# Kernel optimization log

Hardware: AMD Instinct MI355X
Metric: run time of the kernel (lower is better)

Reference implementation:

```python
import jax, jax.numpy as jnp
import numpy as np

N_C = 50000
N_N = 50000
E = 500000
D = 128


def _graph_conv(x_src, src, dst, n_src, n_dst, W, b):
    # DGL GraphConv, norm='both': symmetric degree normalization, then linear.
    ones = jnp.ones(src.shape, x_src.dtype)
    deg_out = jax.ops.segment_sum(ones, src, num_segments=n_src)
    deg_in = jax.ops.segment_sum(ones, dst, num_segments=n_dst)
    norm_src = jnp.maximum(deg_out, 1.0) ** -0.5  # [n_src]
    norm_dst = jnp.maximum(deg_in, 1.0) ** -0.5   # [n_dst]
    m = (x_src * norm_src[:, None])[src]          # [E, D] gather
    agg = jax.ops.segment_sum(m, dst, num_segments=n_dst)  # [n_dst, D]
    return (agg * norm_dst[:, None]) @ W + b


def _sage_conv(x_src, x_dst, src, dst, n_dst, W_self, W_neigh, b):
    # DGL SAGEConv, aggregator='mean': fc_self(h_dst) + fc_neigh(mean_neigh) + bias.
    ones = jnp.ones(src.shape, x_src.dtype)
    deg_in = jnp.maximum(jax.ops.segment_sum(ones, dst, num_segments=n_dst), 1.0)
    h_neigh = jax.ops.segment_sum(x_src[src], dst, num_segments=n_dst) / deg_in[:, None]
    return x_dst @ W_self + h_neigh @ W_neigh + b


def setup_inputs() -> dict:
    key = jax.random.key(0)
    ks = jax.random.split(key, 20)
    s = 1.0 / np.sqrt(D)
    inp = {
        'feat_C': jax.random.normal(ks[0], (N_C, D), jnp.float32),
        'feat_N': jax.random.normal(ks[1], (N_N, D), jnp.float32),
        'W1_cc': jax.random.normal(ks[2], (D, D), jnp.float32) * s,
        'b1_cc': jnp.zeros((D,), jnp.float32),
        'W1_cn': jax.random.normal(ks[3], (D, D), jnp.float32) * s,
        'b1_cn': jnp.zeros((D,), jnp.float32),
        'W1_self': jax.random.normal(ks[4], (D, D), jnp.float32) * s,
        'W1_neigh': jax.random.normal(ks[5], (D, D), jnp.float32) * s,
        'b1_nn': jnp.zeros((D,), jnp.float32),
        'W2_cc': jax.random.normal(ks[6], (D, D), jnp.float32) * s,
        'b2_cc': jnp.zeros((D,), jnp.float32),
        'W2_cn': jax.random.normal(ks[7], (D, D), jnp.float32) * s,
        'b2_cn': jnp.zeros((D,), jnp.float32),
        'W2_self': jax.random.normal(ks[8], (D, D), jnp.float32) * s,
        'W2_neigh': jax.random.normal(ks[9], (D, D), jnp.float32) * s,
        'b2_nn': jnp.zeros((D,), jnp.float32),
        'cc_src': jax.random.randint(ks[10], (E,), 0, N_C),
        'cc_dst': jax.random.randint(ks[11], (E,), 0, N_C),
        'cn_src': jax.random.randint(ks[12], (E,), 0, N_C),
        'cn_dst': jax.random.randint(ks[13], (E,), 0, N_N),
        'nn_src': jax.random.randint(ks[14], (E,), 0, N_N),
        'nn_dst': jax.random.randint(ks[15], (E,), 0, N_N),
    }
    return inp


def reference(feat_C, feat_N, W1_cc, b1_cc, W1_cn, b1_cn, W1_self, W1_neigh, b1_nn,
              W2_cc, b2_cc, W2_cn, b2_cn, W2_self, W2_neigh, b2_nn,
              cc_src, cc_dst, cn_src, cn_dst, nn_src, nn_dst):
    # layer 1 (HeteroGraphConv, aggregate='sum') + relu
    hC = _graph_conv(feat_C, cc_src, cc_dst, N_C, N_C, W1_cc, b1_cc)
    hN = (_graph_conv(feat_C, cn_src, cn_dst, N_C, N_N, W1_cn, b1_cn)
          + _sage_conv(feat_N, feat_N, nn_src, nn_dst, N_N, W1_self, W1_neigh, b1_nn))
    hC = jax.nn.relu(hC)
    hN = jax.nn.relu(hN)
    # layer 2
    oC = _graph_conv(hC, cc_src, cc_dst, N_C, N_C, W2_cc, b2_cc)
    oN = (_graph_conv(hC, cn_src, cn_dst, N_C, N_N, W2_cn, b2_cn)
          + _sage_conv(hN, hN, nn_src, nn_dst, N_N, W2_self, W2_neigh, b2_nn))
    return oC, oN
```

## Files before the change

### kernel.cpp

```cpp
#include <hip/hip_runtime.h>

#define NCN 50000
#define NE  500000
#define DF  128

#define BSHIFT 9
#define NBUCK 98
#define BK 128
#define CAP 7168
#define CHUNK 4096

typedef __attribute__((ext_vector_type(8))) short mfrag;
typedef __attribute__((ext_vector_type(4))) float facc4;

__device__ inline ushort f2bf(float x) {
    unsigned u = __float_as_uint(x);
    unsigned r = (u + 0x7FFFu + ((u >> 16) & 1u)) >> 16;
    return (ushort)r;
}
__device__ inline float bf2f(ushort h) { return __uint_as_float(((unsigned)h) << 16); }

__device__ inline void store_split4m(ushort* __restrict__ T, int row, int lane4,
                                     float4 v, int mode) {
    ushort h0 = f2bf(v.x); ushort l0 = f2bf(v.x - bf2f(h0));
    ushort h1 = f2bf(v.y); ushort l1 = f2bf(v.y - bf2f(h1));
    ushort h2 = f2bf(v.z); ushort l2 = f2bf(v.z - bf2f(h2));
    ushort h3 = f2bf(v.w); ushort l3 = f2bf(v.w - bf2f(h3));
    uint2 hp = make_uint2((uint)h0 | ((uint)h1 << 16), (uint)h2 | ((uint)h3 << 16));
    uint2 lp = make_uint2((uint)l0 | ((uint)l1 << 16), (uint)l2 | ((uint)l3 << 16));
    size_t hiOff, loOff;
    if (mode == 0) { hiOff = (size_t)row * DF; loOff = (size_t)NCN * DF + (size_t)row * DF; }
    else           { hiOff = (size_t)row * 256; loOff = hiOff + 128; }
    *(uint2*)(T + hiOff + lane4 * 4) = hp;
    *(uint2*)(T + loOff + lane4 * 4) = lp;
}

__global__ __launch_bounds__(256) void hist2_k(
    const int* __restrict__ cc_src, const int* __restrict__ cn_src,
    int* __restrict__ cnt2)
{
    int i = blockIdx.x * 256 + threadIdx.x;
    if (i >= NE) return;
    atomicAdd(&cnt2[cc_src[i]], 1);
    atomicAdd(&cnt2[NCN + cn_src[i]], 1);
}

__global__ __launch_bounds__(256) void srcnorm_k(
    const int* __restrict__ cnt2, float* __restrict__ snorm2, int n2)
{
    int i = blockIdx.x * 256 + threadIdx.x;
    if (i >= n2) return;
    int c = cnt2[i]; if (c < 1) c = 1;
    snorm2[i] = rsqrtf((float)c);
}

__global__ __launch_bounds__(256) void binA_k(
    const int* __restrict__ cc_src, const int* __restrict__ cc_dst,
    const int* __restrict__ cn_src, const int* __restrict__ cn_dst,
    const int* __restrict__ nn_src, const int* __restrict__ nn_dst,
    uint2* __restrict__ R, int* __restrict__ bc)
{
    const int s = blockIdx.y;
    const int* key; const int* pay;
    switch (s) {
      case 0: key = cc_dst; pay = cc_src; break;
      case 1: key = cn_dst; pay = cn_src; break;
      default: key = nn_dst; pay = nn_src; break;
    }
    __shared__ uint2 rec[CHUNK];
    __shared__ int lhist[BK], lofs[BK], lcur[BK], gbase[BK];
    __shared__ int ls[256];
    const int tid = threadIdx.x;
    const int base = blockIdx.x * CHUNK;

    int k[16], p[16];
    #pragma unroll
    for (int j = 0; j < 16; ++j) {
        int e = base + j * 256 + tid;
        bool valid = (e < NE);
        k[j] = valid ? key[e] : -1;
        p[j] = valid ? pay[e] : 0;
    }
    if (tid < BK) lhist[tid] = 0;
    __syncthreads();
    #pragma unroll
    for (int j = 0; j < 16; ++j)
        if (k[j] >= 0) atomicAdd(&lhist[k[j] >> BSHIFT], 1);
    __syncthreads();
    int v = (tid < BK) ? lhist[tid] : 0;
    ls[tid] = v;
    __syncthreads();
    #pragma unroll
    for (int off = 1; off < 128; off <<= 1) {
        int t = (tid >= off) ? ls[tid - off] : 0;
        __syncthreads();
        ls[tid] += t;
        __syncthreads();
    }
    if (tid < BK) { int e = ls[tid] - v; lofs[tid] = e; lcur[tid] = e; }
    __syncthreads();
    #pragma unroll
    for (int j = 0; j < 16; ++j) {
        if (k[j] >= 0) {
            int b = k[j] >> BSHIFT;
            int pos = atomicAdd(&lcur[b], 1);
            rec[pos] = make_uint2((unsigned)k[j], (unsigned)p[j]);
        }
    }
    __syncthreads();
    if (tid < BK) {
        int c = lcur[tid] - lofs[tid];
        gbase[tid] = (c > 0) ? atomicAdd(&bc[s * BK + tid], c) : 0;
    }
    __syncthreads();
    int total = ls[127];
    for (int i = tid; i < total; i += 256) {
        uint2 r = rec[i];
        int b = (int)(r.x >> BSHIFT);
        int gi = gbase[b] + (i - lofs[b]);
        R[((size_t)s * NBUCK + b) * CAP + gi] = r;
    }
}

__global__ __launch_bounds__(256) void binB_k(
    const uint2* __restrict__ R, const int* __restrict__ bc,
    int* __restrict__ rp3, int* __restrict__ col3)
{
    const int b = blockIdx.x;
    const int s = blockIdx.y;
    const int tid = threadIdx.x;
    __shared__ int cnt[512];
    __shared__ int lofs[512];
    __shared__ int ls[256];
    __shared__ int sbase;

    const int nrec = bc[s * BK + b];
    const uint2* rec = R + ((size_t)s * NBUCK + b) * CAP;

    for (int i = tid; i < 512; i += 256) cnt[i] = 0;
    __syncthreads();
    for (int i = tid; i < nrec; i += 256)
        atomicAdd(&cnt[rec[i].x & 511], 1);
    __syncthreads();

    {
        int v = (tid < b) ? bc[s * BK + tid] : 0;
        ls[tid] = v;
        __syncthreads();
        for (int off = 128; off > 0; off >>= 1) {
            if (tid < off) ls[tid] += ls[tid + off];
            __syncthreads();
        }
        if (tid == 0) sbase = ls[0];
        __syncthreads();
    }
    const int colBase = sbase;

    int v0 = cnt[2 * tid], v1 = cnt[2 * tid + 1];
    int pairSum = v0 + v1;
    ls[tid] = pairSum;
    __syncthreads();
    #pragma unroll
    for (int off = 1; off < 256; off <<= 1) {
        int t = (tid >= off) ? ls[tid - off] : 0;
        __syncthreads();
        ls[tid] += t;
        __syncthreads();
    }
    int excl = ls[tid] - pairSum;
    lofs[2 * tid] = excl;
    lofs[2 * tid + 1] = excl + v0;
    __syncthreads();
    const int total = ls[255];

    int* rp = rp3 + (size_t)s * (NCN + 1);
    for (int j = tid; j < 512; j += 256) {
        int d = b * 512 + j;
        if (d < NCN) rp[d] = colBase + lofs[j];
    }
    if (b == NBUCK - 1 && tid == 0) rp[NCN] = colBase + total;
    __syncthreads();

    int* col = col3 + (size_t)s * NE + colBase;
    for (int i = tid; i < nrec; i += 256) {
        uint2 r = rec[i];
        int pos = atomicAdd(&lofs[r.x & 511], 1);
        col[pos] = (int)r.y;
    }
}

__global__ __launch_bounds__(256) void wconv_k(
    const float* __restrict__ Wm0, const float* __restrict__ Wm1,
    const float* __restrict__ Wm2, const float* __restrict__ Wm3,
    const float* __restrict__ Wm4, const float* __restrict__ Wm5,
    const float* __restrict__ Wm6, const float* __restrict__ Wm7,
    ushort* __restrict__ out)
{
    const float* Ws[8] = {Wm0, Wm1, Wm2, Wm3, Wm4, Wm5, Wm6, Wm7};
    const float* W = Ws[blockIdx.x];
    ushort* o = out + (size_t)blockIdx.x * 32768;
    for (int i = threadIdx.x; i < 16384; i += 256) {
        int c = i >> 13;
        int r = i & 8191;
        int n = r >> 6;
        int jj = r & 63;
        int kk = c * 64 + (jj ^ ((n & 7) << 3));
        float wv = W[kk * 128 + n];
        ushort h = f2bf(wv);
        float lv = wv - bf2f(h);
        o[c * 16384 + r] = h;
        o[c * 16384 + 8192 + r] = f2bf(lv);
    }
}

__global__ __launch_bounds__(256) void agg_k(
    const float* __restrict__ X0, const int* __restrict__ rp0,
    const int* __restrict__ col0, const float* __restrict__ sc0,
    ushort* __restrict__ out0, int m0,
    const float* __restrict__ X1, const int* __restrict__ rp1,
    const int* __restrict__ col1, const float* __restrict__ sc1,
    ushort* __restrict__ out1, int m1,
    const float* __restrict__ X2, const int* __restrict__ rp2,
    const int* __restrict__ col2, const float* __restrict__ sc2,
    ushort* __restrict__ out2, int m2)
{
    const float* X; const int* rp; const int* col; const float* sc; ushort* out; int mode;
    if (blockIdx.y == 0)      { X = X0; rp = rp0; col = col0; sc = sc0; out = out0; mode = m0; }
    else if (blockIdx.y == 1) { X = X1; rp = rp1; col = col1; sc = sc1; out = out1; mode = m1; }
    else                      { X = X2; rp = rp2; col = col2; sc = sc2; out = out2; mode = m2; }

    int wid = (blockIdx.x * 256 + threadIdx.x) >> 6;
    int half = (threadIdx.x >> 5) & 1;
    int lane4 = threadIdx.x & 31;
    int row = wid * 2 + half;
    if (row >= NCN) return;
    int e0 = rp[row], e1 = rp[row + 1];
    const bool useSc = (sc != nullptr);
    float4 a = make_float4(0.f, 0.f, 0.f, 0.f);
    int e = e0;
    while (e < e1) {
        int cnt = e1 - e; if (cnt > 32) cnt = 32;
        int myc = (lane4 < cnt) ? col[e + lane4] : 0;
        float mysc = (useSc && lane4 < cnt) ? sc[myc] : 1.0f;
        int j = 0;
        for (; j + 4 <= cnt; j += 4) {
            int s0 = __shfl(myc, j, 32),     s1 = __shfl(myc, j + 1, 32);
            int s2 = __shfl(myc, j + 2, 32), s3 = __shfl(myc, j + 3, 32);
            float c0 = __shfl(mysc, j, 32),     c1 = __shfl(mysc, j + 1, 32);
            float c2 = __shfl(mysc, j + 2, 32), c3 = __shfl(mysc, j + 3, 32);
            const float4 u0 = *(const float4*)(X + (size_t)s0 * DF + lane4 * 4);
            const float4 u1 = *(const float4*)(X + (size_t)s1 * DF + lane4 * 4);
            const float4 u2 = *(const float4*)(X + (size_t)s2 * DF + lane4 * 4);
            const float4 u3 = *(const float4*)(X + (size_t)s3 * DF + lane4 * 4);
            a.x = fmaf(u0.x, c0, a.x); a.y = fmaf(u0.y, c0, a.y);
            a.z = fmaf(u0.z, c0, a.z); a.w = fmaf(u0.w, c0, a.w);
            a.x = fmaf(u1.x, c1, a.x); a.y = fmaf(u1.y, c1, a.y);
            a.z = fmaf(u1.z, c1, a.z); a.w = fmaf(u1.w, c1, a.w);
            a.x = fmaf(u2.x, c2, a.x); a.y = fmaf(u2.y, c2, a.y);
            a.z = fmaf(u2.z, c2, a.z); a.w = fmaf(u2.w, c2, a.w);
            a.x = fmaf(u3.x, c3, a.x); a.y = fmaf(u3.y, c3, a.y);
            a.z = fmaf(u3.z, c3, a.z); a.w = fmaf(u3.w, c3, a.w);
        }
        for (; j < cnt; ++j) {
            int s0 = __shfl(myc, j, 32);
            float c0 = __shfl(mysc, j, 32);
            const float4 u0 = *(const float4*)(X + (size_t)s0 * DF + lane4 * 4);
            a.x = fmaf(u0.x, c0, a.x); a.y = fmaf(u0.y, c0, a.y);
            a.z = fmaf(u0.z, c0, a.z); a.w = fmaf(u0.w, c0, a.w);
        }
        e += cnt;
    }
    int deg = e1 - e0; if (deg < 1) deg = 1;
    float dsc = useSc ? rsqrtf((float)deg) : (1.0f / (float)deg);
    a.x *= dsc; a.y *= dsc; a.z *= dsc; a.w *= dsc;
    store_split4m(out, row, lane4, a, mode);
}

template<int NSRC, bool RELU, int F32S, bool A1INT>
__device__ __forceinline__ void gemm_body(
    ushort* __restrict__ Wsm,
    const void* __restrict__ A0, const void* __restrict__ A1, const void* __restrict__ A2,
    const ushort* __restrict__ Wi0, const ushort* __restrict__ Wi1, const ushort* __restrict__ Wi2,
    const float* __restrict__ b0, const float* __restrict__ b1,
    float* __restrict__ Y)
{
    constexpr int NCH = 2 * NSRC;
    const int tid = threadIdx.x;
    const int l = tid & 63;
    const int wv = tid >> 6;
    const int r0 = blockIdx.x * 128;
    const int M = NCN;

    const void*   Aarr[3] = {A0, A1, A2};
    const ushort* Warr[3] = {Wi0, Wi1, Wi2};

    int arow[2];
    #pragma unroll
    for (int rt = 0; rt < 2; ++rt) {
        int r = r0 + wv * 32 + rt * 16 + (l & 15);
        arow[rt] = (r < M) ? r : (M - 1);
    }
    const int kgrp = (l >> 4) * 8;

    facc4 acc[2][8];
    #pragma unroll
    for (int rt = 0; rt < 2; ++rt)
        #pragma unroll
        for (int ct = 0; ct < 8; ++ct)
            acc[rt][ct] = (facc4){0.f, 0.f, 0.f, 0.f};

    uint4 Wr[8];
    auto loadWr = [&](int c) {
        int s = c >> 1, chalf = c & 1;
        const uint4* wp = (const uint4*)(Warr[s] + chalf * 16384);
        #pragma unroll
        for (int i = 0; i < 8; ++i) Wr[i] = wp[i * 256 + tid];
    };

    mfrag ah[2][2], al[2][2];
    auto loadA = [&](int c) {
        int s = c >> 1;
        int k0 = (c & 1) * 64;
        if (s == F32S) {
            const float* F = (const float*)Aarr[s];
            #pragma unroll
            for (int ks = 0; ks < 2; ++ks)
                #pragma unroll
                for (int rt = 0; rt < 2; ++rt) {
                    const float* p = F + (size_t)arow[rt] * DF + k0 + ks * 32 + kgrp;
                    float4 v0 = *(const float4*)p;
                    float4 v1 = *(const float4*)(p + 4);
                    union { mfrag m; ushort u[8]; } H, L;
                    float vv0[4] = {v0.x, v0.y, v0.z, v0.w};
                    float vv1[4] = {v1.x, v1.y, v1.z, v1.w};
                    #pragma unroll
                    for (int j = 0; j < 4; ++j) {
                        ushort h = f2bf(vv0[j]);
                        H.u[j] = h; L.u[j] = f2bf(vv0[j] - bf2f(h));
                    }
                    #pragma unroll
                    for (int j = 0; j < 4; ++j) {
                        ushort h = f2bf(vv1[j]);
                        H.u[4 + j] = h; L.u[4 + j] = f2bf(vv1[j] - bf2f(h));
                    }
                    ah[ks][rt] = H.m; al[ks][rt] = L.m;
                }
        } else {
            const ushort* T = (const ushort*)Aarr[s];
            const bool INT = (s == 1 && A1INT);
            const int rs = INT ? 256 : DF;
            const size_t lo = INT ? 128 : (size_t)NCN * DF;
            #pragma unroll
            for (int ks = 0; ks < 2; ++ks)
                #pragma unroll
                for (int rt = 0; rt < 2; ++rt) {
                    size_t o = (size_t)arow[rt] * rs + k0 + ks * 32 + kgrp;
                    ah[ks][rt] = *(const mfrag*)(T + o);
                    al[ks][rt] = *(const mfrag*)(T + o + lo);
                }
        }
    };

    loadWr(0);
    #pragma unroll
    for (int c = 0; c < NCH; ++c) {
        __syncthreads();
        {
            uint4* wd = (uint4*)Wsm;
            #pragma unroll
            for (int i = 0; i < 8; ++i) wd[i * 256 + tid] = Wr[i];
        }
        loadA(c);
        if (c + 1 < NCH) loadWr(c + 1);
        __syncthreads();
        #pragma unroll
        for (int ks = 0; ks < 2; ++ks) {
            const int kbyte = ks * 64 + (l >> 4) * 16;
            #pragma unroll
            for (int ct = 0; ct < 8; ++ct) {
                int colc = ct * 16 + (l & 15);
                int widx = colc * 64 + ((kbyte ^ ((colc & 7) << 4)) >> 1);
                mfrag w_hi = *(const mfrag*)(Wsm + widx);
                mfrag w_lo = *(const mfrag*)(Wsm + 8192 + widx);
                #pragma unroll
                for (int rt = 0; rt < 2; ++rt) {
                    acc[rt][ct] = __builtin_amdgcn_mfma_f32_16x16x32_bf16(ah[ks][rt], w_hi, acc[rt][ct], 0, 0, 0);
                    acc[rt][ct] = __builtin_amdgcn_mfma_f32_16x16x32_bf16(ah[ks][rt], w_lo, acc[rt][ct], 0, 0, 0);
                    acc[rt][ct] = __builtin_amdgcn_mfma_f32_16x16x32_bf16(al[ks][rt], w_hi, acc[rt][ct], 0, 0, 0);
                }
            }
        }
    }
    __syncthreads();

    float bias[8];
    #pragma unroll
    for (int ct = 0; ct < 8; ++ct) {
        int colc = ct * 16 + (l & 15);
        float bv = b0 ? b0[colc] : 0.f;
        if (b1) bv += b1[colc];
        bias[ct] = bv;
    }
    #pragma unroll
    for (int rt = 0; rt < 2; ++rt) {
        #pragma unroll
        for (int q = 0; q < 4; ++q) {
            int row = r0 + wv * 32 + rt * 16 + (l >> 4) * 4 + q;
            if (row < M) {
                #pragma unroll
                for (int ct = 0; ct < 8; ++ct) {
                    float v = acc[rt][ct][q] + bias[ct];
                    if (RELU) v = fmaxf(v, 0.f);
                    Y[(size_t)row * DF + ct * 16 + (l & 15)] = v;
                }
            }
        }
    }
}

template<bool RELU>
__global__ __launch_bounds__(256, 2) void fgemm2_k(
    const ushort* __restrict__ AN0, const ushort* __restrict__ AN1i,
    const float* __restrict__ AN2f,
    const ushort* __restrict__ WiN0, const ushort* __restrict__ WiN1,
    const ushort* __restrict__ WiN2,
    const float* __restrict__ bN0, const float* __restrict__ bN1,
    float* __restrict__ YN,
    const ushort* __restrict__ AC0, const ushort* __restrict__ WiC,
    const float* __restrict__ bC, float* __restrict__ YC)
{
    __shared__ ushort Wsm[16384];
    if (blockIdx.z == 0)
        gemm_body<3, RELU, 2, true>(Wsm, AN0, AN1i, AN2f, WiN0, WiN1, WiN2,
                                    bN0, bN1, YN);
    else
        gemm_body<1, RELU, -1, false>(Wsm, AC0, nullptr, nullptr,
                                      WiC, nullptr, nullptr, bC, nullptr, YC);
}

template<bool RELU>
__global__ __launch_bounds__(256, 2) void gemmN_k(
    const ushort* __restrict__ A0, const ushort* __restrict__ A1i,
    const float* __restrict__ A2f,
    const ushort* __restrict__ Wi0, const ushort* __restrict__ Wi1,
    const ushort* __restrict__ Wi2,
    const float* __restrict__ b0, const float* __restrict__ b1,
    float* __restrict__ Y)
{
    __shared__ ushort Wsm[16384];
    gemm_body<3, RELU, 2, true>(Wsm, A0, A1i, A2f, Wi0, Wi1, Wi2, b0, b1, Y);
}

template<bool RELU>
__global__ __launch_bounds__(256, 2) void gemmC_k(
    const ushort* __restrict__ A0, const ushort* __restrict__ Wi0,
    const float* __restrict__ b0, float* __restrict__ Y)
{
    __shared__ ushort Wsm[16384];
    gemm_body<1, RELU, -1, false>(Wsm, A0, nullptr, nullptr, Wi0, nullptr, nullptr,
                                  b0, nullptr, Y);
}

extern "C" void kernel_launch(void* const* d_in, const int* in_sizes, int n_in,
                              void* d_out, int out_size, void* d_ws, size_t ws_size,
                              hipStream_t stream)
{
    (void)in_sizes; (void)n_in; (void)out_size; (void)ws_size;
    const float* feat_C   = (const float*)d_in[0];
    const float* feat_N   = (const float*)d_in[1];
    const float* W1_cc    = (const float*)d_in[2];
    const float* b1_cc    = (const float*)d_in[3];
    const float* W1_cn    = (const float*)d_in[4];
    const float* b1_cn    = (const float*)d_in[5];
    const float* W1_self  = (const float*)d_in[6];
    const float* W1_neigh = (const float*)d_in[7];
    const float* b1_nn    = (const float*)d_in[8];
    const float* W2_cc    = (const float*)d_in[9];
    const float* b2_cc    = (const float*)d_in[10];
    const float* W2_cn    = (const float*)d_in[11];
    const float* b2_cn    = (const float*)d_in[12];
    const float* W2_self  = (const float*)d_in[13];
    const float* W2_neigh = (const float*)d_in[14];
    const float* b2_nn    = (const float*)d_in[15];
    const int* cc_src = (const int*)d_in[16];
    const int* cc_dst = (const int*)d_in[17];
    const int* cn_src = (const int*)d_in[18];
    const int* cn_dst = (const int*)d_in[19];
    const int* nn_src = (const int*)d_in[20];
    const int* nn_dst = (const int*)d_in[21];

    char* ws = (char*)d_ws;
    size_t off = 0;
    auto take = [&](size_t bytes) -> char* {
        char* p = ws + off;
        off = (off + bytes + 255) & ~(size_t)255;
        return p;
    };
    int*    rp3    = (int*)take((size_t)3 * (NCN + 1) * sizeof(int));
    int*    col3   = (int*)take((size_t)3 * NE * sizeof(int));
    float*  snorm2 = (float*)take((size_t)2 * NCN * sizeof(float));
    int*    cnt2   = (int*)take((size_t)2 * NCN * sizeof(int));
    int*    bc     = (int*)take((size_t)3 * BK * sizeof(int));
    ushort* Wimg   = (ushort*)take((size_t)8 * 32768 * sizeof(ushort));
    char* bigRegion = take((size_t)2 * 2 * NCN * DF * sizeof(ushort));
    uint2*  R  = (uint2*)bigRegion;
    ushort* P0 = (ushort*)bigRegion;
    ushort* P1 = (ushort*)(bigRegion + (size_t)2 * NCN * DF * sizeof(ushort));

    float* oC = (float*)d_out;
    float* oN = oC + (size_t)NCN * DF;
    ushort* oC_us = (ushort*)oC;
    ushort* oN_us = (ushort*)oN;

    const int edgeBlocks = (NE + 255) / 256;
    const int binABlocks = (NE + CHUNK - 1) / CHUNK;
    const int aggBlocks  = (((NCN + 1) / 2) * 64 + 255) / 256;
    const int gemmBlocks = (NCN + 127) / 128;

    auto img = [&](int m) { return (const ushort*)(Wimg + (size_t)m * 32768); };
    const int* rpCC = rp3 + 0 * (NCN + 1);
    const int* rpCN = rp3 + 1 * (NCN + 1);
    const int* rpNN = rp3 + 2 * (NCN + 1);
    const int* colCC = col3 + 0 * NE;
    const int* colCN = col3 + 1 * NE;
    const int* colNN = col3 + 2 * NE;
    const float* snCC = snorm2 + 0 * NCN;
    const float* snCN = snorm2 + 1 * NCN;

    hipMemsetAsync(cnt2, 0, (size_t)2 * NCN * sizeof(int), stream);
    hipMemsetAsync(bc, 0, (size_t)3 * BK * sizeof(int), stream);
    hist2_k<<<edgeBlocks, 256, 0, stream>>>(cc_src, cn_src, cnt2);
    srcnorm_k<<<(2 * NCN + 255) / 256, 256, 0, stream>>>(cnt2, snorm2, 2 * NCN);
    binA_k<<<dim3(binABlocks, 3), 256, 0, stream>>>(cc_src, cc_dst, cn_src, cn_dst,
                                                    nn_src, nn_dst, R, bc);
    binB_k<<<dim3(NBUCK, 3), 256, 0, stream>>>(R, bc, rp3, col3);
    wconv_k<<<8, 256, 0, stream>>>(W1_cc, W1_cn, W1_neigh, W1_self,
                                   W2_cc, W2_cn, W2_neigh, W2_self, Wimg);

    agg_k<<<dim3(aggBlocks, 3), 256, 0, stream>>>(
        feat_C, rpCC, colCC, snCC, P0, 0,
        feat_C, rpCN, colCN, snCN, P1, 0,
        feat_N, rpNN, colNN, nullptr, oN_us, 1);
    fgemm2_k<true><<<dim3(gemmBlocks, 1, 2), 256, 0, stream>>>(
        P1, oN_us, feat_N, img(1), img(2), img(3), b1_cn, b1_nn, oN,
        P0, img(0), b1_cc, oC);

    agg_k<<<dim3(aggBlocks, 2), 256, 0, stream>>>(
        oC, rpCC, colCC, snCC, P0, 0,
        oC, rpCN, colCN, snCN, P1, 0,
        nullptr, nullptr, nullptr, nullptr, nullptr, 0);
    agg_k<<<dim3(aggBlocks, 1), 256, 0, stream>>>(
        oN, rpNN, colNN, nullptr, oC_us, 1,
        nullptr, nullptr, nullptr, nullptr, nullptr, 0,
        nullptr, nullptr, nullptr, nullptr, nullptr, 0);
    gemmN_k<false><<<gemmBlocks, 256, 0, stream>>>(P1, oC_us, oN,
                                                   img(5), img(6), img(7),
                                                   b2_cn, b2_nn, oN);
    gemmC_k<false><<<gemmBlocks, 256, 0, stream>>>(P0, img(4), b2_cc, oC);
}
```

Measured before the change: 425.7 us.

## Use a third workspace table to fuse layer-2 aggregations and GEMMs

When the workspace has room, the neighbour-mean aggregation for the NN relation is written to a separate P2 buffer instead of aliasing the output. Layer 2 can then run all three aggregations in one launch and both GEMMs in one fused launch, cutting the launch count from four to two. Launch bounds on the GEMM kernels also rise from 2 to 3 blocks per CU, which can force register spilling. The extra buffer costs workspace memory, and the old path is kept as a fallback.

```diff
diff --git a/kernel.cpp b/kernel.cpp
--- a/kernel.cpp
+++ b/kernel.cpp
@@ -418,9 +418,9 @@
     }
 }
 
-template<bool RELU>
-__global__ __launch_bounds__(256, 2) void fgemm2_k(
-    const ushort* __restrict__ AN0, const ushort* __restrict__ AN1i,
+template<bool RELU, bool A1INT>
+__global__ __launch_bounds__(256, 3) void fgemm2_k(
+    const ushort* __restrict__ AN0, const ushort* __restrict__ AN1,
     const float* __restrict__ AN2f,
     const ushort* __restrict__ WiN0, const ushort* __restrict__ WiN1,
     const ushort* __restrict__ WiN2,
@@ -431,15 +431,15 @@
 {
     __shared__ ushort Wsm[16384];
     if (blockIdx.z == 0)
-        gemm_body<3, RELU, 2, true>(Wsm, AN0, AN1i, AN2f, WiN0, WiN1, WiN2,
-                                    bN0, bN1, YN);
+        gemm_body<3, RELU, 2, A1INT>(Wsm, AN0, AN1, AN2f, WiN0, WiN1, WiN2,
+                                     bN0, bN1, YN);
     else
         gemm_body<1, RELU, -1, false>(Wsm, AC0, nullptr, nullptr,
                                       WiC, nullptr, nullptr, bC, nullptr, YC);
 }
 
 template<bool RELU>
-__global__ __launch_bounds__(256, 2) void gemmN_k(
+__global__ __launch_bounds__(256, 3) void gemmN_k(
     const ushort* __restrict__ A0, const ushort* __restrict__ A1i,
     const float* __restrict__ A2f,
     const ushort* __restrict__ Wi0, const ushort* __restrict__ Wi1,
@@ -452,7 +452,7 @@
 }
 
 template<bool RELU>
-__global__ __launch_bounds__(256, 2) void gemmC_k(
+__global__ __launch_bounds__(256, 3) void gemmC_k(
     const ushort* __restrict__ A0, const ushort* __restrict__ Wi0,
     const float* __restrict__ b0, float* __restrict__ Y)
 {
@@ -465,7 +465,7 @@
                               void* d_out, int out_size, void* d_ws, size_t ws_size,
                               hipStream_t stream)
 {
-    (void)in_sizes; (void)n_in; (void)out_size; (void)ws_size;
+    (void)in_sizes; (void)n_in; (void)out_size;
     const float* feat_C   = (const float*)d_in[0];
     const float* feat_N   = (const float*)d_in[1];
     const float* W1_cc    = (const float*)d_in[2];
@@ -496,16 +496,19 @@
         off = (off + bytes + 255) & ~(size_t)255;
         return p;
     };
+    const size_t TBL = (size_t)2 * NCN * DF * sizeof(ushort);
     int*    rp3    = (int*)take((size_t)3 * (NCN + 1) * sizeof(int));
     int*    col3   = (int*)take((size_t)3 * NE * sizeof(int));
     float*  snorm2 = (float*)take((size_t)2 * NCN * sizeof(float));
     int*    cnt2   = (int*)take((size_t)2 * NCN * sizeof(int));
     int*    bc     = (int*)take((size_t)3 * BK * sizeof(int));
     ushort* Wimg   = (ushort*)take((size_t)8 * 32768 * sizeof(ushort));
-    char* bigRegion = take((size_t)2 * 2 * NCN * DF * sizeof(ushort));
+    char* bigRegion = take(2 * TBL);
     uint2*  R  = (uint2*)bigRegion;
     ushort* P0 = (ushort*)bigRegion;
-    ushort* P1 = (ushort*)(bigRegion + (size_t)2 * NCN * DF * sizeof(ushort));
+    ushort* P1 = (ushort*)(bigRegion + TBL);
+    const bool useP2 = (ws_size >= off + TBL);
+    ushort* P2 = useP2 ? (ushort*)take(TBL) : nullptr;
 
     float* oC = (float*)d_out;
     float* oN = oC + (size_t)NCN * DF;
@@ -537,24 +540,40 @@
     wconv_k<<<8, 256, 0, stream>>>(W1_cc, W1_cn, W1_neigh, W1_self,
                                    W2_cc, W2_cn, W2_neigh, W2_self, Wimg);
 
-    agg_k<<<dim3(aggBlocks, 3), 256, 0, stream>>>(
-        feat_C, rpCC, colCC, snCC, P0, 0,
-        feat_C, rpCN, colCN, snCN, P1, 0,
-        feat_N, rpNN, colNN, nullptr, oN_us, 1);
-    fgemm2_k<true><<<dim3(gemmBlocks, 1, 2), 256, 0, stream>>>(
-        P1, oN_us, feat_N, img(1), img(2), img(3), b1_cn, b1_nn, oN,
-        P0, img(0), b1_cc, oC);
-
-    agg_k<<<dim3(aggBlocks, 2), 256, 0, stream>>>(
-        oC, rpCC, colCC, snCC, P0, 0,
-        oC, rpCN, colCN, snCN, P1, 0,
-        nullptr, nullptr, nullptr, nullptr, nullptr, 0);
-    agg_k<<<dim3(aggBlocks, 1), 256, 0, stream>>>(
-        oN, rpNN, colNN, nullptr, oC_us, 1,
-        nullptr, nullptr, nullptr, nullptr, nullptr, 0,
-        nullptr, nullptr, nullptr, nullptr, nullptr, 0);
-    gemmN_k<false><<<gemmBlocks, 256, 0, stream>>>(P1, oC_us, oN,
-                                                   img(5), img(6), img(7),
-                                                   b2_cn, b2_nn, oN);
-    gemmC_k<false><<<gemmBlocks, 256, 0, stream>>>(P0, img(4), b2_cc, oC);
-}
+    if (useP2) {
+        agg_k<<<dim3(aggBlocks, 3), 256, 0, stream>>>(
+            feat_C, rpCC, colCC, snCC, P0, 0,
+            feat_C, rpCN, colCN, snCN, P1, 0,
+            feat_N, rpNN, colNN, nullptr, P2, 0);
+        fgemm2_k<true, false><<<dim3(gemmBlocks, 1, 2), 256, 0, stream>>>(
+            P1, P2, feat_N, img(1), img(2), img(3), b1_cn, b1_nn, oN,
+            P0, img(0), b1_cc, oC);
+        agg_k<<<dim3(aggBlocks, 3), 256, 0, stream>>>(
+            oC, rpCC, colCC, snCC, P0, 0,
+            oC, rpCN, colCN, snCN, P1, 0,
+            oN, rpNN, colNN, nullptr, P2, 0);
+        fgemm2_k<false, false><<<dim3(gemmBlocks, 1, 2), 256, 0, stream>>>(
+            P1, P2, oN, img(5), img(6), img(7), b2_cn, b2_nn, oN,
+            P0, img(4), b2_cc, oC);
+    } else {
+        agg_k<<<dim3(aggBlocks, 3), 256, 0, stream>>>(
+            feat_C, rpCC, colCC, snCC, P0, 0,
+            feat_C, rpCN, colCN, snCN, P1, 0,
+            feat_N, rpNN, colNN, nullptr, oN_us, 1);
+        fgemm2_k<true, true><<<dim3(gemmBlocks, 1, 2), 256, 0, stream>>>(
+            P1, oN_us, feat_N, img(1), img(2), img(3), b1_cn, b1_nn, oN,
+            P0, img(0), b1_cc, oC);
+        agg_k<<<dim3(aggBlocks, 2), 256, 0, stream>>>(
+            oC, rpCC, colCC, snCC, P0, 0,
+            oC, rpCN, colCN, snCN, P1, 0,
+            nullptr, nullptr, nullptr, nullptr, nullptr, 0);
+        agg_k<<<dim3(aggBlocks, 1), 256, 0, stream>>>(
+            oN, rpNN, colNN, nullptr, oC_us, 1,
+            nullptr, nullptr, nullptr, nullptr, nullptr, 0,
+            nullptr, nullptr, nullptr, nullptr, nullptr, 0);
+        gemmN_k<false><<<gemmBlocks, 256, 0, stream>>>(P1, oC_us, oN,
+                                                       img(5), img(6), img(7),
+                                                       b2_cn, b2_nn, oN);
+        gemmC_k<false><<<gemmBlocks, 256, 0, stream>>>(P0, img(4), b2_cc, oC);
+    }
+}
```

Measured after the change: 432.4 us. About the same (+1.6%).
